# Performance work log

Hardware: AMD Instinct MI355X
Metric: run time of the kernel (lower is better)

Reference implementation:

```python
import jax, jax.numpy as jnp
import numpy as np

B, N = 1, 512
NODE_DIM, EDGE_DIM = 384, 128
H, SK, SV, PK, PV = 8, 16, 16, 4, 4
EPS = 1e-8
LN_EPS = 1e-5


def setup_inputs() -> dict:
    key = jax.random.key(0)
    ks = jax.random.split(key, 20)
    d, e = NODE_DIM, EDGE_DIM
    s = 0.02
    rn = lambda k, sh: jax.random.normal(k, sh, jnp.float32) * s
    # orthonormal per-residue rotations (valid rigid frames)
    R, _ = jnp.linalg.qr(jax.random.normal(ks[2], (B, N, 3, 3), jnp.float32))
    out_dim = H * (SV + EDGE_DIM + PV * 4)  # scalar + pairwise + points(3) + point norms(1)
    return dict(
        node_features=jax.random.normal(ks[0], (B, N, d), jnp.float32),
        edge_features=jax.random.normal(ks[1], (B, N, N, e), jnp.float32),
        rotations=R,
        translations=jax.random.normal(ks[3], (B, N, 3), jnp.float32),
        mask=jnp.ones((B, N), bool),
        Wq_s=rn(ks[4], (d, H * SK)), Wk_s=rn(ks[5], (d, H * SK)), Wv_s=rn(ks[6], (d, H * SV)),
        Wq_p=rn(ks[7], (d, H * PK * 3)), Wk_p=rn(ks[8], (d, H * PK * 3)), Wv_p=rn(ks[9], (d, H * PV * 3)),
        point_weights=jnp.full((H,), np.log(np.e - 1.0), jnp.float32),  # softplus -> 1
        Wb=rn(ks[10], (e, H)), bb=jnp.zeros((H,), jnp.float32),
        Wo=rn(ks[11], (out_dim, d)), bo=jnp.zeros((d,), jnp.float32),
        g1=jnp.ones((d,), jnp.float32), beta1=jnp.zeros((d,), jnp.float32),
        W1=rn(ks[12], (d, 2 * d)), b1=jnp.zeros((2 * d,), jnp.float32),
        W2=rn(ks[13], (2 * d, 2 * d)), b2=jnp.zeros((2 * d,), jnp.float32),
        W3=rn(ks[14], (2 * d, d)), b3=jnp.zeros((d,), jnp.float32),
        g2=jnp.ones((d,), jnp.float32), beta2=jnp.zeros((d,), jnp.float32),
    )


def _layer_norm(x, g, b):
    mu = x.mean(-1, keepdims=True)
    var = ((x - mu) ** 2).mean(-1, keepdims=True)
    return (x - mu) * jax.lax.rsqrt(var + LN_EPS) * g + b


def _forward(node_features, edge_features, rotations, translations, mask,
             Wq_s, Wk_s, Wv_s, Wq_p, Wk_p, Wv_p, point_weights, Wb, bb, Wo, bo,
             g1, beta1, W1, b1, W2, b2, W3, b3, g2, beta2):
    b, n, d = node_features.shape
    # num_attn_logits = 3 (scalar + point + pairwise)
    scal_scale = (3 * SK) ** -0.5
    point_scale = (3 * PK * 4.5) ** -0.5
    pair_scale = 3 ** -0.5

    qs = (node_features @ Wq_s).reshape(b, n, H, SK)
    kk = (node_features @ Wk_s).reshape(b, n, H, SK)
    vs = (node_features @ Wv_s).reshape(b, n, H, SV)

    def apply_rigid(p):  # p: (b,n,h,d,3); global = R^T applied per lucidrains einsum + t
        return jnp.einsum('bnhdc,bncr->bnhdr', p, rotations) + translations[:, :, None, None, :]

    qp = apply_rigid((node_features @ Wq_p).reshape(b, n, H, PK, 3))
    kp = apply_rigid((node_features @ Wk_p).reshape(b, n, H, PK, 3))
    vp = apply_rigid((node_features @ Wv_p).reshape(b, n, H, PV, 3))

    logits = jnp.einsum('bihk,bjhk->bhij', qs, kk) * scal_scale

    # point distance term: sum_{d,c} (q-k)^2 = |q|^2 + |k|^2 - 2 q.k (avoids (b,h,i,j,d,3) tensor)
    w = jax.nn.softplus(point_weights)  # (H,)
    q2 = jnp.einsum('bnhdc,bnhdc->bhn', qp, qp)
    k2 = jnp.einsum('bnhdc,bnhdc->bhn', kp, kp)
    cross = jnp.einsum('bihdc,bjhdc->bhij', qp, kp)
    dist = q2[..., :, None] + k2[..., None, :] - 2.0 * cross  # (b,h,i,j)
    logits = logits - 0.5 * point_scale * w[None, :, None, None] * dist

    pair_bias = (jnp.einsum('bije,eh->bhij', edge_features, Wb) + bb[None, :, None, None]) * pair_scale
    logits = logits + pair_bias

    pm = mask[:, None, :, None] & mask[:, None, None, :]  # (b,1,i,j)
    logits = jnp.where(pm, logits, -jnp.finfo(logits.dtype).max)
    attn = jax.nn.softmax(logits, axis=-1)  # (b,h,i,j)

    rs = jnp.einsum('bhij,bjhv->bihv', attn, vs).reshape(b, n, H * SV)
    rp = jnp.einsum('bhij,bije->bihe', attn, edge_features).reshape(b, n, H * EDGE_DIM)
    pts = jnp.einsum('bhij,bjhdc->bihdc', attn, vp)
    # invert rigid: subtract t, apply R (inverse of R^T application)
    local = jnp.einsum('bihdc,birc->bihdr', pts - translations[:, :, None, None, :], rotations)
    norms = jnp.sqrt((local ** 2).sum(-1) + EPS)  # (b,n,H,PV)

    cat = jnp.concatenate([rs, local.reshape(b, n, H * PV * 3), norms.reshape(b, n, H * PV), rp], axis=-1)
    ipa_out = cat @ Wo + bo

    x = _layer_norm(ipa_out, g1, beta1)  # dropout is identity at eval
    x = jax.nn.relu(x @ W1 + b1)
    x = jax.nn.relu(x @ W2 + b2)
    x = x @ W3 + b3
    return _layer_norm(x, g2, beta2)


def reference(node_features, edge_features, rotations, translations, mask,
              Wq_s, Wk_s, Wv_s, Wq_p, Wk_p, Wv_p, point_weights, Wb, bb, Wo, bo,
              g1, beta1, W1, b1, W2, b2, W3, b3, g2, beta2):
    return _forward(node_features, edge_features, rotations, translations, mask,
                    Wq_s, Wk_s, Wv_s, Wq_p, Wk_p, Wv_p, point_weights, Wb, bb, Wo, bo,
                    g1, beta1, W1, b1, W2, b2, W3, b3, g2, beta2)
```

## Files before the change

kernel.cpp:

```cpp
#include <hip/hip_runtime.h>
#include <cstddef>

#define NN 512
#define DD 384
#define EE 128
#define HH 8
#define JSPLIT 16

static constexpr float SCAL_SCALE  = 0.1443375673f;
static constexpr float POINT_SCALE = 0.1360827635f;
static constexpr float PAIR_SCALE  = 0.5773502692f;
static constexpr float LN_EPS = 1e-5f;
static constexpr float EPS    = 1e-8f;

typedef __bf16 bf16x8 __attribute__((ext_vector_type(8)));
typedef float  f32x4  __attribute__((ext_vector_type(4)));

__device__ __forceinline__ unsigned short bf16_bits(float v) {
    union { __bf16 b; unsigned short s; } c; c.b = (__bf16)v; return c.s;
}
__device__ __forceinline__ float bits2f(unsigned u) {
    union { unsigned u; float f; } c; c.u = u; return c.f;
}

__global__ __launch_bounds__(256) void prep_weights_kernel(
    const float* __restrict__ Wo, const float* __restrict__ W1,
    const float* __restrict__ W2, const float* __restrict__ W3,
    const float* __restrict__ Wq_s, const float* __restrict__ Wk_s,
    const float* __restrict__ Wv_s,
    const float* __restrict__ Wq_p, const float* __restrict__ Wk_p,
    const float* __restrict__ Wv_p, const float* __restrict__ nf,
    unsigned short* __restrict__ WoT, unsigned short* __restrict__ W1T,
    unsigned short* __restrict__ W2T, unsigned short* __restrict__ W3T,
    unsigned short* __restrict__ WprojT, unsigned short* __restrict__ nfb)
{
    const int b = blockIdx.x;
    if (b >= 1884) {
        const int idx = (b - 1884) * 1024 + threadIdx.x * 4;
        float4 v = *(const float4*)(nf + idx);
        unsigned lo = bf16_bits(v.x) | ((unsigned)bf16_bits(v.y) << 16);
        unsigned hi = bf16_bits(v.z) | ((unsigned)bf16_bits(v.w) << 16);
        uint2 pk; pk.x = lo; pk.y = hi;
        *(uint2*)(nfb + idx) = pk;
        return;
    }
    const float* W; unsigned short* out;
    int K, N, tile, rowoff = 0;
    if (b < 480)       { W = Wo;   out = WoT;    K = 1280; N = 384; tile = b; }
    else if (b < 768)  { W = W1;   out = W1T;    K = 384;  N = 768; tile = b - 480; }
    else if (b < 1344) { W = W2;   out = W2T;    K = 768;  N = 768; tile = b - 768; }
    else if (b < 1632) { W = W3;   out = W3T;    K = 768;  N = 384; tile = b - 1344; }
    else if (b < 1680) { W = Wq_s; out = WprojT; K = 384;  N = 128; tile = b - 1632; rowoff = 0; }
    else if (b < 1728) { W = Wk_s; out = WprojT; K = 384;  N = 128; tile = b - 1680; rowoff = 128; }
    else if (b < 1776) { W = Wv_s; out = WprojT; K = 384;  N = 128; tile = b - 1728; rowoff = 256; }
    else if (b < 1812) { W = Wq_p; out = WprojT; K = 384;  N = 96;  tile = b - 1776; rowoff = 384; }
    else if (b < 1848) { W = Wk_p; out = WprojT; K = 384;  N = 96;  tile = b - 1812; rowoff = 480; }
    else               { W = Wv_p; out = WprojT; K = 384;  N = 96;  tile = b - 1848; rowoff = 576; }

    const int ntn = N / 32;
    const int n0 = (tile % ntn) * 32, k0 = (tile / ntn) * 32;
    __shared__ float tb[32][33];
    const int tx = threadIdx.x & 31, ty = threadIdx.x >> 5;
    #pragma unroll
    for (int dy = 0; dy < 32; dy += 8)
        tb[ty + dy][tx] = W[(size_t)(k0 + ty + dy) * N + n0 + tx];
    __syncthreads();
    #pragma unroll
    for (int dy = 0; dy < 32; dy += 8)
        out[(size_t)(rowoff + n0 + ty + dy) * K + k0 + tx] = bf16_bits(tb[tx][ty + dy]);
}

template <int K, int NOUT, bool RELU, bool HASB, bool OUTBF>
__global__ __launch_bounds__(256) void gemm_bf16(
    const unsigned short* __restrict__ Xb, const unsigned short* __restrict__ Wt,
    const float* __restrict__ bias, void* __restrict__ Yv)
{
    const int t = threadIdx.x;
    const int w = t >> 6, lane = t & 63;
    const int r = lane & 15, q = lane >> 4;
    const int mt = w >> 1, kh = w & 1;
    const int n0 = blockIdx.x * 16;
    const int m0 = blockIdx.y * 32 + mt * 16;
    constexpr int KH = K / 2;

    const unsigned short* xrow = Xb + (size_t)(m0 + r) * K + kh * KH + q * 8;
    const unsigned short* wrow = Wt + (size_t)(n0 + r) * K + kh * KH + q * 8;

    f32x4 acc = {0.f, 0.f, 0.f, 0.f};
    #pragma unroll 4
    for (int k0 = 0; k0 < KH; k0 += 32) {
        union { uint4 u; bf16x8 v; } au, bu;
        au.u = *(const uint4*)(xrow + k0);
        bu.u = *(const uint4*)(wrow + k0);
        acc = __builtin_amdgcn_mfma_f32_16x16x32_bf16(au.v, bu.v, acc, 0, 0, 0);
    }

    __shared__ float red[2][16][17];
    if (kh == 1) {
        #pragma unroll
        for (int reg = 0; reg < 4; reg++)
            red[mt][q * 4 + reg][r] = acc[reg];
    }
    __syncthreads();
    if (kh == 1) return;

    const int n = n0 + r;
    const float bi = HASB ? bias[n] : 0.f;
    #pragma unroll
    for (int reg = 0; reg < 4; reg++) {
        const int m = m0 + q * 4 + reg;
        float v = acc[reg] + red[mt][q * 4 + reg][r] + bi;
        if (RELU) v = fmaxf(v, 0.f);
        if (OUTBF) ((unsigned short*)Yv)[(size_t)m * NOUT + n] = bf16_bits(v);
        else       ((float*)Yv)[(size_t)m * NOUT + n] = v;
    }
}

__global__ __launch_bounds__(256) void ipa_post_kernel(
    const float* __restrict__ proj_out, const float* __restrict__ rot,
    const float* __restrict__ trans, const float* __restrict__ pw,
    const float* __restrict__ bb,
    unsigned short* __restrict__ Qp, unsigned short* __restrict__ Kp,
    unsigned short* __restrict__ svT)
{
    const int i = blockIdx.x;
    const int t = threadIdx.x;
    __shared__ float outs[672];
    __shared__ float ptg[288];
    __shared__ float q2s[8], k2s[8], pwh[8];

    for (int f = t; f < 672; f += 256) outs[f] = proj_out[(size_t)i * 672 + f];
    if (t < 8) pwh[t] = 0.5f * POINT_SCALE * log1pf(expf(pw[t]));
    __syncthreads();

    for (int f = t; f < 288; f += 256) {
        int which = f / 96, idx = f % 96;
        int hd = idx / 3, r = idx % 3;
        float acc = trans[(size_t)i * 3 + r];
        #pragma unroll
        for (int c = 0; c < 3; c++)
            acc += outs[384 + which * 96 + hd * 3 + c] * rot[(size_t)i * 9 + c * 3 + r];
        ptg[f] = acc;
    }
    __syncthreads();
    if (t < 16) {
        int which = t / 8, h = t % 8;
        float acc = 0.f;
        #pragma unroll
        for (int m = 0; m < 12; m++) {
            float v = ptg[which * 96 + h * 12 + m];
            acc += v * v;
        }
        (which ? k2s : q2s)[h] = acc;
    }
    __syncthreads();

    {
        const int h = t >> 5, d = t & 31;
        float qv, kv;
        if (d < 16)      { qv = outs[h * 16 + d] * SCAL_SCALE; kv = outs[128 + h * 16 + d]; }
        else if (d < 28) { qv = ptg[h * 12 + d - 16] * (2.f * pwh[h]); kv = ptg[96 + h * 12 + d - 16]; }
        else if (d == 28){ qv = -pwh[h] * q2s[h]; kv = 1.f; }
        else if (d == 29){ qv = 1.f; kv = -pwh[h] * k2s[h]; }
        else if (d == 30){ qv = 1.f; kv = bb[h] * PAIR_SCALE; }
        else             { qv = 0.f; kv = 0.f; }
        Qp[((size_t)i * 8 + h) * 32 + d] = bf16_bits(qv);
        Kp[((size_t)i * 8 + h) * 32 + d] = bf16_bits(kv);
    }
    if (t < 128) {
        int h = t >> 4, v = t & 15;
        svT[((size_t)h * 32 + v) * NN + i] = bf16_bits(outs[256 + h * 16 + v]);
    } else if (t < 224) {
        int idx = t - 128, h = idx / 12, m = idx % 12;
        svT[((size_t)h * 32 + 16 + m) * NN + i] = bf16_bits(ptg[192 + idx]);
    } else {
        int idx = t - 224;
        int h = idx >> 2, m = 28 + (idx & 3);
        svT[((size_t)h * 32 + m) * NN + i] = 0;
    }
}

__global__ __launch_bounds__(256) void ipa_fused2(
    const float* __restrict__ edge,
    const unsigned short* __restrict__ Qp, const unsigned short* __restrict__ Kp,
    const unsigned short* __restrict__ svT, const float* __restrict__ Wb,
    float* __restrict__ Opart, float* __restrict__ Mpart, float* __restrict__ Lpart)
{
    const int js = blockIdx.x;
    const int it = blockIdx.y;
    const int i0 = it * 8;
    const int jbase = js * 32;
    const int t = threadIdx.x;
    const int w = t >> 6, lane = t & 63;
    const int r = lane & 15, q = lane >> 4;

    __shared__ float Lqk[64 * 33];
    __shared__ __align__(16) unsigned short P1[72 * 32];
    __shared__ __align__(16) unsigned short P2[72 * 32];
    __shared__ __align__(16) unsigned short wbTl[8 * 136];
    __shared__ __align__(16) unsigned short eT[4 * 128 * 32];

    if (t < 128) {
        float4 a = *(const float4*)&Wb[t * 8];
        float4 b = *(const float4*)&Wb[t * 8 + 4];
        wbTl[0 * 136 + t] = bf16_bits(a.x * PAIR_SCALE);
        wbTl[1 * 136 + t] = bf16_bits(a.y * PAIR_SCALE);
        wbTl[2 * 136 + t] = bf16_bits(a.z * PAIR_SCALE);
        wbTl[3 * 136 + t] = bf16_bits(a.w * PAIR_SCALE);
        wbTl[4 * 136 + t] = bf16_bits(b.x * PAIR_SCALE);
        wbTl[5 * 136 + t] = bf16_bits(b.y * PAIR_SCALE);
        wbTl[6 * 136 + t] = bf16_bits(b.z * PAIR_SCALE);
        wbTl[7 * 136 + t] = bf16_bits(b.w * PAIR_SCALE);
    }

    const int te = t >> 1, th8 = t & 1;
    float pf[4][16];

    auto issue_pf = [&](int half) {
        #pragma unroll
        for (int k = 0; k < 4; k++) {
            const float* src = edge + (((size_t)(i0 + half * 4 + k) * 512 + jbase + th8 * 16) * 128) + te;
            #pragma unroll
            for (int s = 0; s < 16; s++) pf[k][s] = src[(size_t)s * 128];
        }
    };
    auto commit_pf = [&]() {
        #pragma unroll
        for (int k = 0; k < 4; k++) {
            union { uint4 u2[2]; unsigned short sh[16]; } pk;
            #pragma unroll
            for (int s = 0; s < 16; s++) pk.sh[s] = bf16_bits(pf[k][s]);
            unsigned short* dst = &eT[k * 4096 + te * 32];
            *(uint4*)(dst + (((2 * th8)     ^ (te & 3)) * 8)) = pk.u2[0];
            *(uint4*)(dst + (((2 * th8 + 1) ^ (te & 3)) * 8)) = pk.u2[1];
        }
    };

    bf16x8 aq[2]; bf16x8 bk[2][2];
    #pragma unroll
    for (int hh = 0; hh < 2; hh++) {
        const int h = w * 2 + hh;
        aq[hh] = *(const bf16x8*)&Qp[((size_t)(i0 + (r & 7)) * 8 + h) * 32 + q * 8];
        #pragma unroll
        for (int jt = 0; jt < 2; jt++)
            bk[hh][jt] = *(const bf16x8*)&Kp[((size_t)(jbase + jt * 16 + r) * 8 + h) * 32 + q * 8];
    }

    issue_pf(0);

    #pragma unroll
    for (int hh = 0; hh < 2; hh++) {
        const int h = w * 2 + hh;
        #pragma unroll
        for (int jt = 0; jt < 2; jt++) {
            f32x4 acc = {0.f, 0.f, 0.f, 0.f};
            acc = __builtin_amdgcn_mfma_f32_16x16x32_bf16(aq[hh], bk[hh][jt], acc, 0, 0, 0);
            if (q < 2) {
                #pragma unroll
                for (int reg = 0; reg < 4; reg++)
                    Lqk[(h * 8 + q * 4 + reg) * 33 + jt * 16 + r] = acc[reg];
            }
        }
    }
    __syncthreads();

    #pragma unroll
    for (int half = 0; half < 2; half++) {
        {
            const int il = half * 4 + w;
            const float* ebase = edge + ((size_t)(i0 + il) * 512 + jbase) * 128;
            #pragma unroll
            for (int jt = 0; jt < 2; jt++) {
                f32x4 acc = {0.f, 0.f, 0.f, 0.f};
                #pragma unroll
                for (int kk = 0; kk < 4; kk++) {
                    const float* srcb = ebase + (size_t)(jt * 16 + r) * 128 + kk * 32 + q * 8;
                    float4 f0 = *(const float4*)srcb;
                    float4 f1 = *(const float4*)(srcb + 4);
                    union { uint4 u; bf16x8 v; } aE;
                    aE.u.x = (unsigned)bf16_bits(f0.x) | ((unsigned)bf16_bits(f0.y) << 16);
                    aE.u.y = (unsigned)bf16_bits(f0.z) | ((unsigned)bf16_bits(f0.w) << 16);
                    aE.u.z = (unsigned)bf16_bits(f1.x) | ((unsigned)bf16_bits(f1.y) << 16);
                    aE.u.w = (unsigned)bf16_bits(f1.z) | ((unsigned)bf16_bits(f1.w) << 16);
                    union { uint4 u; bf16x8 v; } bW;
                    bW.u = *(const uint4*)&wbTl[(r & 7) * 136 + kk * 32 + q * 8];
                    acc = __builtin_amdgcn_mfma_f32_16x16x32_bf16(aE.v, bW.v, acc, 0, 0, 0);
                }
                if (r < 8) {
                    #pragma unroll
                    for (int reg = 0; reg < 4; reg++)
                        Lqk[(r * 8 + il) * 33 + jt * 16 + q * 4 + reg] += acc[reg];
                }
            }
        }
        commit_pf();
        if (half == 0) issue_pf(1);
        __syncthreads();

        if (t < 32) {
            const int h = t >> 2, il = half * 4 + (t & 3);
            const float* lrow = &Lqk[(h * 8 + il) * 33];
            float lg[32];
            float mx = -1e30f;
            #pragma unroll
            for (int j = 0; j < 32; j++) {
                lg[j] = lrow[j];
                mx = fmaxf(mx, lg[j]);
            }
            float sum = 0.f;
            #pragma unroll
            for (int j = 0; j < 32; j++) { lg[j] = __expf(lg[j] - mx); sum += lg[j]; }
            Mpart[(size_t)(js * 64 + it) * 64 + h * 8 + il] = mx;
            Lpart[(size_t)(js * 64 + it) * 64 + h * 8 + il] = sum;
            unsigned pk[16];
            #pragma unroll
            for (int s = 0; s < 16; s++)
                pk[s] = (unsigned)bf16_bits(lg[2 * s]) | ((unsigned)bf16_bits(lg[2 * s + 1]) << 16);
            uint4* d1 = (uint4*)&P1[((size_t)il * 8 + h) * 32];
            uint4* d2 = (uint4*)&P2[((size_t)h * 8 + il) * 32];
            #pragma unroll
            for (int s = 0; s < 4; s++) {
                uint4 v; v.x = pk[4*s]; v.y = pk[4*s+1]; v.z = pk[4*s+2]; v.w = pk[4*s+3];
                d1[s] = v; d2[s] = v;
            }
        }
        __syncthreads();

        {
            const int il = half * 4 + w;
            union { uint4 u; bf16x8 v; } bP;
            bP.u = *(const uint4*)&P1[((size_t)il * 8 + r) * 32 + q * 8];
            union { uint4 u; bf16x8 v; } aF[8];
            #pragma unroll
            for (int eb = 0; eb < 8; eb++)
                aF[eb].u = *(const uint4*)&eT[w * 4096 + (eb * 16 + r) * 32 + ((q ^ (r & 3)) * 8)];
            f32x4 acc[8];
            #pragma unroll
            for (int eb = 0; eb < 8; eb++) {
                f32x4 c = {0.f, 0.f, 0.f, 0.f};
                acc[eb] = __builtin_amdgcn_mfma_f32_16x16x32_bf16(aF[eb].v, bP.v, c, 0, 0, 0);
            }
            float* orw = Opart + (size_t)((js * 64 + it) * 8 + il) * 1248;
            if (r < 8) {
                #pragma unroll
                for (int eb = 0; eb < 8; eb++)
                    *(f32x4*)&orw[r * 156 + 28 + eb * 16 + q * 4] = acc[eb];
            }
        }
        if (half == 0) __syncthreads();
    }

    #pragma unroll
    for (int hh = 0; hh < 2; hh++) {
        const int h = w * 2 + hh;
        union { uint4 u; bf16x8 v; } aP;
        aP.u = *(const uint4*)&P2[((size_t)h * 8 + r) * 32 + q * 8];
        #pragma unroll
        for (int ct = 0; ct < 2; ct++) {
            union { uint4 u; bf16x8 v; } bS;
            bS.u = *(const uint4*)&svT[((size_t)h * 32 + ct * 16 + r) * 512 + jbase + q * 8];
            f32x4 c = {0.f, 0.f, 0.f, 0.f};
            f32x4 acc = __builtin_amdgcn_mfma_f32_16x16x32_bf16(aP.v, bS.v, c, 0, 0, 0);
            const int cc = ct * 16 + r;
            if (q < 2 && cc < 28) {
                #pragma unroll
                for (int reg = 0; reg < 4; reg++) {
                    const int i = q * 4 + reg;
                    Opart[((size_t)((js * 64 + it) * 8 + i)) * 1248 + h * 156 + cc] = acc[reg];
                }
            }
        }
    }
}

__global__ __launch_bounds__(256) void ipa_merge(
    const float* __restrict__ Opart, const float* __restrict__ Mpart,
    const float* __restrict__ Lpart, const float* __restrict__ rot,
    const float* __restrict__ trans, unsigned short* __restrict__ cat_bf)
{
    const int i = blockIdx.x;
    const int itile = i >> 3, il = i & 7;
    const int t = threadIdx.x;
    __shared__ float wn[8 * JSPLIT];
    __shared__ float pts_s[96];

    if (t < 8) {
        const int h = t;
        float ms[JSPLIT], ls[JSPLIT], M = -1e30f;
        #pragma unroll
        for (int s = 0; s < JSPLIT; s++) {
            ms[s] = Mpart[(size_t)(s * 64 + itile) * 64 + h * 8 + il];
            ls[s] = Lpart[(size_t)(s * 64 + itile) * 64 + h * 8 + il];
            M = fmaxf(M, ms[s]);
        }
        float denom = 0.f, e[JSPLIT];
        #pragma unroll
        for (int s = 0; s < JSPLIT; s++) { e[s] = __expf(ms[s] - M); denom += e[s] * ls[s]; }
        const float inv = 1.f / denom;
        #pragma unroll
        for (int s = 0; s < JSPLIT; s++) wn[h * JSPLIT + s] = e[s] * inv;
    }
    __syncthreads();

    for (int col = t; col < 1248; col += 256) {
        const int h = col / 156, c = col % 156;
        float acc = 0.f;
        #pragma unroll
        for (int s = 0; s < JSPLIT; s++)
            acc += wn[h * JSPLIT + s] *
                   Opart[((size_t)(s * 64 + itile) * 8 + il) * 1248 + col];
        if (c < 16)      cat_bf[(size_t)i * 1280 + h * 16 + c] = bf16_bits(acc);
        else if (c < 28) pts_s[h * 12 + (c - 16)] = acc;
        else             cat_bf[(size_t)i * 1280 + 256 + h * 128 + (c - 28)] = bf16_bits(acc);
    }
    __syncthreads();

    const float* tr = trans + (size_t)i * 3;
    const float* R  = rot + (size_t)i * 9;
    if (t < 96) {
        int hd = t / 3, rr = t % 3;
        float acc = 0.f;
        #pragma unroll
        for (int c = 0; c < 3; c++)
            acc += (pts_s[hd * 3 + c] - tr[c]) * R[rr * 3 + c];
        cat_bf[(size_t)i * 1280 + 128 + t] = bf16_bits(acc);
    } else if (t < 128) {
        int pv = t - 96;
        float s = EPS;
        #pragma unroll
        for (int rr = 0; rr < 3; rr++) {
            float v = 0.f;
            #pragma unroll
            for (int c = 0; c < 3; c++)
                v += (pts_s[pv * 3 + c] - tr[c]) * R[rr * 3 + c];
            s += v * v;
        }
        cat_bf[(size_t)i * 1280 + 224 + pv] = bf16_bits(sqrtf(s));
    }
}

template <bool OUTBF>
__global__ __launch_bounds__(256) void ln_kernel(
    const float* __restrict__ X, const float* __restrict__ g,
    const float* __restrict__ beta, void* __restrict__ Yv, int Dim)
{
    __shared__ float red[4];
    __shared__ float bc;
    const int i = blockIdx.x;
    const int t = threadIdx.x;
    const float* x = X + (size_t)i * Dim;

    float s = 0.f;
    for (int k = t; k < Dim; k += 256) s += x[k];
    #pragma unroll
    for (int off = 32; off; off >>= 1) s += __shfl_down(s, off, 64);
    if ((t & 63) == 0) red[t >> 6] = s;
    __syncthreads();
    if (t == 0) bc = red[0] + red[1] + red[2] + red[3];
    __syncthreads();
    const float mu = bc / Dim;

    float v = 0.f;
    for (int k = t; k < Dim; k += 256) { float d = x[k] - mu; v += d * d; }
    #pragma unroll
    for (int off = 32; off; off >>= 1) v += __shfl_down(v, off, 64);
    __syncthreads();
    if ((t & 63) == 0) red[t >> 6] = v;
    __syncthreads();
    if (t == 0) bc = red[0] + red[1] + red[2] + red[3];
    __syncthreads();
    const float rstd = rsqrtf(bc / Dim + LN_EPS);

    for (int k = t; k < Dim; k += 256) {
        float val = (x[k] - mu) * rstd * g[k] + beta[k];
        if (OUTBF) ((unsigned short*)Yv)[(size_t)i * Dim + k] = bf16_bits(val);
        else       ((float*)Yv)[(size_t)i * Dim + k] = val;
    }
}

extern "C" void kernel_launch(void* const* d_in, const int* in_sizes, int n_in,
                              void* d_out, int out_size, void* d_ws, size_t ws_size,
                              hipStream_t stream)
{
    const float* nf    = (const float*)d_in[0];
    const float* edge  = (const float*)d_in[1];
    const float* rot   = (const float*)d_in[2];
    const float* trans = (const float*)d_in[3];
    const float* Wq_s = (const float*)d_in[5];
    const float* Wk_s = (const float*)d_in[6];
    const float* Wv_s = (const float*)d_in[7];
    const float* Wq_p = (const float*)d_in[8];
    const float* Wk_p = (const float*)d_in[9];
    const float* Wv_p = (const float*)d_in[10];
    const float* pw   = (const float*)d_in[11];
    const float* Wb   = (const float*)d_in[12];
    const float* bb   = (const float*)d_in[13];
    const float* Wo   = (const float*)d_in[14];
    const float* bo   = (const float*)d_in[15];
    const float* g1   = (const float*)d_in[16];
    const float* be1  = (const float*)d_in[17];
    const float* W1   = (const float*)d_in[18];
    const float* b1   = (const float*)d_in[19];
    const float* W2   = (const float*)d_in[20];
    const float* b2   = (const float*)d_in[21];
    const float* W3   = (const float*)d_in[22];
    const float* b3   = (const float*)d_in[23];
    const float* g2   = (const float*)d_in[24];
    const float* be2  = (const float*)d_in[25];

    float* ws = (float*)d_ws;
    float* proj_out = ws;
    float* ipa   = proj_out + 344064;
    float* y     = ipa + 196608;
    float* Opart = y + 196608;
    float* Mpart = Opart + 10223616;
    float* Lpart = Mpart + 65536;
    unsigned short* cat_bf = (unsigned short*)(Lpart + 65536);
    unsigned short* x1b = cat_bf + 655360;
    unsigned short* h1b = x1b + 196608;
    unsigned short* h2b = h1b + 393216;
    unsigned short* Qp  = h2b + 393216;
    unsigned short* Kp  = Qp + 131072;
    unsigned short* svT = Kp + 131072;
    unsigned short* WoT = svT + 131072;
    unsigned short* W1T = WoT + 491520;
    unsigned short* W2T = W1T + 294912;
    unsigned short* W3T = W2T + 589824;
    unsigned short* WprojT = W3T + 294912;
    unsigned short* nfb = WprojT + 258048;

    prep_weights_kernel<<<2076, 256, 0, stream>>>(Wo, W1, W2, W3,
                                                  Wq_s, Wk_s, Wv_s, Wq_p, Wk_p, Wv_p, nf,
                                                  WoT, W1T, W2T, W3T, WprojT, nfb);

    gemm_bf16<384, 672, false, false, false><<<dim3(42, 16), 256, 0, stream>>>(nfb, WprojT, nullptr, proj_out);

    ipa_post_kernel<<<NN, 256, 0, stream>>>(proj_out, rot, trans, pw, bb, Qp, Kp, svT);

    ipa_fused2<<<dim3(JSPLIT, 64), 256, 0, stream>>>(edge, Qp, Kp, svT, Wb,
                                                     Opart, Mpart, Lpart);

    ipa_merge<<<NN, 256, 0, stream>>>(Opart, Mpart, Lpart, rot, trans, cat_bf);

    gemm_bf16<1280, 384, false, true, false><<<dim3(24, 16), 256, 0, stream>>>(cat_bf, WoT, bo, ipa);
    ln_kernel<true><<<NN, 256, 0, stream>>>(ipa, g1, be1, x1b, 384);

    gemm_bf16<384, 768, true, true, true><<<dim3(48, 16), 256, 0, stream>>>(x1b, W1T, b1, h1b);
    gemm_bf16<768, 768, true, true, true><<<dim3(48, 16), 256, 0, stream>>>(h1b, W2T, b2, h2b);
    gemm_bf16<768, 384, false, true, false><<<dim3(24, 16), 256, 0, stream>>>(h2b, W3T, b3, y);

    ln_kernel<false><<<NN, 256, 0, stream>>>(y, g2, be2, d_out, 384);
}
```

Baseline: 327.9 us.

## Load edge tile with per-warp float2 rows and pad LDS transpose buffer

```diff
diff --git a/kernel.cpp b/kernel.cpp
--- a/kernel.cpp
+++ b/kernel.cpp
@@ -193,12 +193,13 @@
     const int t = threadIdx.x;
     const int w = t >> 6, lane = t & 63;
     const int r = lane & 15, q = lane >> 4;
+    const int L = lane;
 
     __shared__ float Lqk[64 * 33];
     __shared__ __align__(16) unsigned short P1[72 * 32];
     __shared__ __align__(16) unsigned short P2[72 * 32];
     __shared__ __align__(16) unsigned short wbTl[8 * 136];
-    __shared__ __align__(16) unsigned short eT[4 * 128 * 32];
+    __shared__ __align__(16) unsigned short eT[4 * 128 * 40];
 
     if (t < 128) {
         float4 a = *(const float4*)&Wb[t * 8];
@@ -213,26 +214,26 @@
         wbTl[7 * 136 + t] = bf16_bits(b.w * PAIR_SCALE);
     }
 
-    const int te = t >> 1, th8 = t & 1;
-    float pf[4][16];
+    float2 pf[32];
 
     auto issue_pf = [&](int half) {
-        #pragma unroll
-        for (int k = 0; k < 4; k++) {
-            const float* src = edge + (((size_t)(i0 + half * 4 + k) * 512 + jbase + th8 * 16) * 128) + te;
-            #pragma unroll
-            for (int s = 0; s < 16; s++) pf[k][s] = src[(size_t)s * 128];
-        }
+        const float* src = edge + ((size_t)(i0 + half * 4 + w) * 512 + jbase) * 128 + 2 * L;
+        #pragma unroll
+        for (int s = 0; s < 32; s++)
+            pf[s] = *(const float2*)(src + (size_t)s * 128);
     };
     auto commit_pf = [&]() {
         #pragma unroll
-        for (int k = 0; k < 4; k++) {
-            union { uint4 u2[2]; unsigned short sh[16]; } pk;
-            #pragma unroll
-            for (int s = 0; s < 16; s++) pk.sh[s] = bf16_bits(pf[k][s]);
-            unsigned short* dst = &eT[k * 4096 + te * 32];
-            *(uint4*)(dst + (((2 * th8)     ^ (te & 3)) * 8)) = pk.u2[0];
-            *(uint4*)(dst + (((2 * th8 + 1) ^ (te & 3)) * 8)) = pk.u2[1];
+        for (int c = 0; c < 2; c++) {
+            #pragma unroll
+            for (int jb = 0; jb < 4; jb++) {
+                union { uint4 u; unsigned short sh[8]; } pk;
+                #pragma unroll
+                for (int u2 = 0; u2 < 8; u2++)
+                    pk.sh[u2] = bf16_bits(c ? pf[jb * 8 + u2].y : pf[jb * 8 + u2].x);
+                const int jseg = (jb + (L >> 2)) & 3;
+                *(uint4*)&eT[w * 5120 + (2 * L + c) * 40 + jseg * 8] = pk.u;
+            }
         }
     };
 
@@ -332,8 +333,10 @@
             bP.u = *(const uint4*)&P1[((size_t)il * 8 + r) * 32 + q * 8];
             union { uint4 u; bf16x8 v; } aF[8];
             #pragma unroll
-            for (int eb = 0; eb < 8; eb++)
-                aF[eb].u = *(const uint4*)&eT[w * 4096 + (eb * 16 + r) * 32 + ((q ^ (r & 3)) * 8)];
+            for (int eb = 0; eb < 8; eb++) {
+                const int jseg = (q + 2 * eb + (r >> 3)) & 3;
+                aF[eb].u = *(const uint4*)&eT[w * 5120 + (eb * 16 + r) * 40 + jseg * 8];
+            }
             f32x4 acc[8];
             #pragma unroll
             for (int eb = 0; eb < 8; eb++) {
@@ -347,7 +350,6 @@
                     *(f32x4*)&orw[r * 156 + 28 + eb * 16 + q * 4] = acc[eb];
             }
         }
-        if (half == 0) __syncthreads();
     }
 
     #pragma unroll
```

Measured after the change: 325.6 us, median of 2. About the same (-0.7%).
